# Performance work log

Measured on AMD Instinct MI355X. Metric: run time of the kernel, lower is better.

## Reference

```python
import jax, jax.numpy as jnp
import numpy as np
import math

N_EMBD = 1024
N_HEAD = 16
B, T = 2, 2048


def new_gelu(x):
    # GPT-2 tanh-approx GELU (matches torch module exactly)
    return 0.5 * x * (1.0 + jnp.tanh(jnp.sqrt(2.0 / jnp.pi) * (x + 0.044715 * x ** 3)))


def layer_norm(x, w, b, eps=1e-5):
    mu = jnp.mean(x, axis=-1, keepdims=True)
    var = jnp.var(x, axis=-1, keepdims=True)
    return (x - mu) * jax.lax.rsqrt(var + eps) * w + b


def setup_inputs() -> dict:
    key = jax.random.key(0)
    ks = jax.random.split(key, 8)
    C = N_EMBD
    s = 0.02
    return {
        "x": jax.random.normal(ks[0], (B, T, C), dtype=jnp.float32),
        "ln1_w": jnp.ones((C,), jnp.float32),
        "ln1_b": jnp.zeros((C,), jnp.float32),
        "attn_w": s * jax.random.normal(ks[1], (C, 3 * C), jnp.float32),
        "attn_b": jnp.zeros((3 * C,), jnp.float32),
        "attn_proj_w": s * jax.random.normal(ks[2], (C, C), jnp.float32),
        "attn_proj_b": jnp.zeros((C,), jnp.float32),
        "ln2_w": jnp.ones((C,), jnp.float32),
        "ln2_b": jnp.zeros((C,), jnp.float32),
        "fc_w": s * jax.random.normal(ks[3], (C, 4 * C), jnp.float32),
        "fc_b": jnp.zeros((4 * C,), jnp.float32),
        "mlp_proj_w": s * jax.random.normal(ks[4], (4 * C, C), jnp.float32),
        "mlp_proj_b": jnp.zeros((C,), jnp.float32),
    }


def block_forward(x, ln1_w, ln1_b, attn_w, attn_b, attn_proj_w, attn_proj_b,
                  ln2_w, ln2_b, fc_w, fc_b, mlp_proj_w, mlp_proj_b):
    Bm, Tm, C = x.shape
    H = N_HEAD
    D = C // H
    # --- self attention (pre-LN) ---
    h = layer_norm(x, ln1_w, ln1_b)
    qkv = h @ attn_w + attn_b  # [B,T,3C]
    q, k, v = jnp.split(qkv, 3, axis=-1)
    q = q.reshape(Bm, Tm, H, D).transpose(0, 2, 1, 3)  # [B,H,T,D]
    k = k.reshape(Bm, Tm, H, D).transpose(0, 2, 1, 3)
    v = v.reshape(Bm, Tm, H, D).transpose(0, 2, 1, 3)
    att = jnp.einsum('bhqd,bhkd->bhqk', q, k) * (1.0 / math.sqrt(D))
    att = jax.nn.softmax(att, axis=-1)  # NOTE: no causal mask in source
    y = jnp.einsum('bhqk,bhkd->bhqd', att, v)
    y = y.transpose(0, 2, 1, 3).reshape(Bm, Tm, C)
    x = x + (y @ attn_proj_w + attn_proj_b)
    # --- MLP ---
    h = layer_norm(x, ln2_w, ln2_b)
    h = new_gelu(h @ fc_w + fc_b)
    x = x + (h @ mlp_proj_w + mlp_proj_b)
    return x


def reference(x, ln1_w, ln1_b, attn_w, attn_b, attn_proj_w, attn_proj_b,
              ln2_w, ln2_b, fc_w, fc_b, mlp_proj_w, mlp_proj_b):
    return block_forward(x, ln1_w, ln1_b, attn_w, attn_b, attn_proj_w, attn_proj_b,
                         ln2_w, ln2_b, fc_w, fc_b, mlp_proj_w, mlp_proj_b)
```

## Files before the change

### kernel.cpp

```cpp
#include <hip/hip_runtime.h>

typedef __attribute__((ext_vector_type(4))) float  f32x4;
typedef __attribute__((ext_vector_type(8))) short  s16x8;
typedef __attribute__((ext_vector_type(4))) short  s16x4;

__device__ __forceinline__ short f2bf(float f) {
    unsigned u = __builtin_bit_cast(unsigned, f);
    u += 0x7fff + ((u >> 16) & 1);
    return (short)(u >> 16);
}

__device__ __forceinline__ void load_lds16(const void* g, void* l) {
    __builtin_amdgcn_global_load_lds(
        (const __attribute__((address_space(1))) unsigned int*)g,
        (__attribute__((address_space(3))) unsigned int*)l, 16, 0, 0);
}

__global__ __launch_bounds__(256) void transpose_cast(const float* __restrict__ W,
                                                      short* __restrict__ Wt,
                                                      int K, int N) {
    __shared__ float t[32][33];
    int n0 = blockIdx.x * 32, k0 = blockIdx.y * 32;
    int tx = threadIdx.x & 31, ty = threadIdx.x >> 5;
#pragma unroll
    for (int i = 0; i < 4; i++)
        t[ty + 8 * i][tx] = W[(size_t)(k0 + ty + 8 * i) * N + n0 + tx];
    __syncthreads();
#pragma unroll
    for (int i = 0; i < 4; i++)
        Wt[(size_t)(n0 + ty + 8 * i) * K + k0 + tx] = f2bf(t[tx][ty + 8 * i]);
}

__global__ __launch_bounds__(256) void vtrans_kernel(const short* __restrict__ qkv,
                                                     short* __restrict__ Vtg) {
    const int T = 2048, C3 = 3072;
    __shared__ short tl[32][33];
    int bh = blockIdx.y >> 1;
    int b = bh >> 4, h = bh & 15;
    int dh = (blockIdx.y & 1) * 32;
    int t0 = blockIdx.x * 32;
    int tx = threadIdx.x & 31, ty = threadIdx.x >> 5;
    const short* src = qkv + (size_t)b * T * C3 + 2048 + h * 64 + dh;
#pragma unroll
    for (int i = 0; i < 4; i++)
        tl[ty + 8 * i][tx] = src[(size_t)(t0 + ty + 8 * i) * C3 + tx];
    __syncthreads();
#pragma unroll
    for (int i = 0; i < 4; i++)
        Vtg[((size_t)bh * 64 + dh + ty + 8 * i) * T + t0 + tx] = tl[tx][ty + 8 * i];
}

__global__ __launch_bounds__(256) void ln_kernel(const float* __restrict__ x,
                                                 const float* __restrict__ w,
                                                 const float* __restrict__ b,
                                                 short* __restrict__ out) {
    int row = blockIdx.x;
    int tid = threadIdx.x;
    const float4 v = ((const float4*)(x + (size_t)row * 1024))[tid];
    float s  = v.x + v.y + v.z + v.w;
    float ss = v.x * v.x + v.y * v.y + v.z * v.z + v.w * v.w;
#pragma unroll
    for (int o = 32; o > 0; o >>= 1) {
        s  += __shfl_down(s, o);
        ss += __shfl_down(ss, o);
    }
    __shared__ float rs[4], rq[4];
    int wave = tid >> 6, lane = tid & 63;
    if (lane == 0) { rs[wave] = s; rq[wave] = ss; }
    __syncthreads();
    float tot = rs[0] + rs[1] + rs[2] + rs[3];
    float tq  = rq[0] + rq[1] + rq[2] + rq[3];
    float mu   = tot * (1.f / 1024.f);
    float var  = tq * (1.f / 1024.f) - mu * mu;
    float rstd = rsqrtf(var + 1e-5f);
    const float4 wv = ((const float4*)w)[tid];
    const float4 bv = ((const float4*)b)[tid];
    s16x4 o;
    o[0] = f2bf((v.x - mu) * rstd * wv.x + bv.x);
    o[1] = f2bf((v.y - mu) * rstd * wv.y + bv.y);
    o[2] = f2bf((v.z - mu) * rstd * wv.z + bv.z);
    o[3] = f2bf((v.w - mu) * rstd * wv.w + bv.w);
    ((s16x4*)(out + (size_t)row * 1024))[tid] = o;
}

template <typename OUT_T, bool GELU, bool RES, bool SCALE_Q>
__global__ __launch_bounds__(256) void gemm_bt(const short* __restrict__ A,
                                               const short* __restrict__ Bt,
                                               const float* __restrict__ bias,
                                               const float* __restrict__ res,
                                               OUT_T* __restrict__ C,
                                               int M, int N, int K) {
    __shared__ __align__(16) short As[128 * 32];
    __shared__ __align__(16) short Bs[128 * 32];
    int tid = threadIdx.x;
    int m0 = blockIdx.y * 128, n0 = blockIdx.x * 128;
    int wave = tid >> 6, lane = tid & 63;
    int wr = wave >> 1, wc = wave & 1;
    int g = lane >> 4, q = lane & 15;
    f32x4 acc[4][4] = {};
    const short* Ab = A + (size_t)m0 * K;
    const short* Bb = Bt + (size_t)n0 * K;
    int srow = tid >> 2;
    int scol = (tid & 3) * 8;
    for (int k0 = 0; k0 < K; k0 += 32) {
        __syncthreads();
        load_lds16(Ab + (size_t)srow * K + k0 + scol, As + tid * 8);
        load_lds16(Ab + (size_t)(srow + 64) * K + k0 + scol, As + 2048 + tid * 8);
        load_lds16(Bb + (size_t)srow * K + k0 + scol, Bs + tid * 8);
        load_lds16(Bb + (size_t)(srow + 64) * K + k0 + scol, Bs + 2048 + tid * 8);
        __syncthreads();
        s16x8 a[4], bf[4];
#pragma unroll
        for (int mi = 0; mi < 4; mi++)
            a[mi] = *(const s16x8*)(As + (wr * 64 + mi * 16 + q) * 32 + g * 8);
#pragma unroll
        for (int ni = 0; ni < 4; ni++)
            bf[ni] = *(const s16x8*)(Bs + (wc * 64 + ni * 16 + q) * 32 + g * 8);
#pragma unroll
        for (int mi = 0; mi < 4; mi++)
#pragma unroll
            for (int ni = 0; ni < 4; ni++)
                acc[mi][ni] = __builtin_amdgcn_mfma_f32_16x16x32_bf16(a[mi], bf[ni], acc[mi][ni], 0, 0, 0);
    }
#pragma unroll
    for (int mi = 0; mi < 4; mi++) {
#pragma unroll
        for (int ni = 0; ni < 4; ni++) {
            int row = m0 + wr * 64 + mi * 16 + g * 4;
            int col = n0 + wc * 64 + ni * 16 + q;
            float bb = bias[col];
#pragma unroll
            for (int r = 0; r < 4; r++) {
                float v = acc[mi][ni][r] + bb;
                if (RES) v += res[(size_t)(row + r) * N + col];
                if (GELU) {
                    float aa = 0.7978845608028654f * (v + 0.044715f * v * v * v);
                    float th = 1.f - 2.f / (__expf(2.f * aa) + 1.f);
                    v = 0.5f * v * (1.f + th);
                }
                if (SCALE_Q && col < 1024) v *= 0.18033688011112042f;
                if constexpr (sizeof(OUT_T) == 2)
                    C[(size_t)(row + r) * N + col] = f2bf(v);
                else
                    C[(size_t)(row + r) * N + col] = v;
            }
        }
    }
}

__global__ __launch_bounds__(256) void gemm_bt_sk(const short* __restrict__ A,
                                                  const short* __restrict__ Bt,
                                                  float* __restrict__ part,
                                                  int M, int N, int K, int Klen) {
    __shared__ __align__(16) short As[128 * 32];
    __shared__ __align__(16) short Bs[128 * 32];
    int tid = threadIdx.x;
    int m0 = blockIdx.y * 128, n0 = blockIdx.x * 128;
    int kz = blockIdx.z;
    int wave = tid >> 6, lane = tid & 63;
    int wr = wave >> 1, wc = wave & 1;
    int g = lane >> 4, q = lane & 15;
    f32x4 acc[4][4] = {};
    const short* Ab = A + (size_t)m0 * K;
    const short* Bb = Bt + (size_t)n0 * K;
    int srow = tid >> 2;
    int scol = (tid & 3) * 8;
    int kend = kz * Klen + Klen;
    for (int k0 = kz * Klen; k0 < kend; k0 += 32) {
        __syncthreads();
        load_lds16(Ab + (size_t)srow * K + k0 + scol, As + tid * 8);
        load_lds16(Ab + (size_t)(srow + 64) * K + k0 + scol, As + 2048 + tid * 8);
        load_lds16(Bb + (size_t)srow * K + k0 + scol, Bs + tid * 8);
        load_lds16(Bb + (size_t)(srow + 64) * K + k0 + scol, Bs + 2048 + tid * 8);
        __syncthreads();
        s16x8 a[4], bf[4];
#pragma unroll
        for (int mi = 0; mi < 4; mi++)
            a[mi] = *(const s16x8*)(As + (wr * 64 + mi * 16 + q) * 32 + g * 8);
#pragma unroll
        for (int ni = 0; ni < 4; ni++)
            bf[ni] = *(const s16x8*)(Bs + (wc * 64 + ni * 16 + q) * 32 + g * 8);
#pragma unroll
        for (int mi = 0; mi < 4; mi++)
#pragma unroll
            for (int ni = 0; ni < 4; ni++)
                acc[mi][ni] = __builtin_amdgcn_mfma_f32_16x16x32_bf16(a[mi], bf[ni], acc[mi][ni], 0, 0, 0);
    }
    float* pb = part + (size_t)kz * M * N;
#pragma unroll
    for (int mi = 0; mi < 4; mi++) {
#pragma unroll
        for (int ni = 0; ni < 4; ni++) {
            int row = m0 + wr * 64 + mi * 16 + g * 4;
            int col = n0 + wc * 64 + ni * 16 + q;
#pragma unroll
            for (int r = 0; r < 4; r++)
                pb[(size_t)(row + r) * N + col] = acc[mi][ni][r];
        }
    }
}

template <int SK>
__global__ __launch_bounds__(256) void reduce_sk(const float* __restrict__ part,
                                                 const float* __restrict__ bias,
                                                 const float* __restrict__ res,
                                                 float* __restrict__ out,
                                                 int MN, int N) {
    int tot = MN >> 2;
    int nb4 = (N >> 2) - 1;
    for (int i = blockIdx.x * 256 + threadIdx.x; i < tot; i += gridDim.x * 256) {
        float4 s = ((const float4*)part)[i];
#pragma unroll
        for (int k = 1; k < SK; k++) {
            float4 p = ((const float4*)(part + (size_t)k * MN))[i];
            s.x += p.x; s.y += p.y; s.z += p.z; s.w += p.w;
        }
        float4 bv = ((const float4*)bias)[i & nb4];
        float4 rv = ((const float4*)res)[i];
        float4 o;
        o.x = s.x + bv.x + rv.x;
        o.y = s.y + bv.y + rv.y;
        o.z = s.z + bv.z + rv.z;
        o.w = s.w + bv.w + rv.w;
        ((float4*)out)[i] = o;
    }
}

__global__ __launch_bounds__(256) void attn_kernel(const short* __restrict__ qkv,
                                                   const short* __restrict__ Vtg,
                                                   short* __restrict__ y) {
    const int T = 2048, C3 = 3072;
    int wg = blockIdx.x;
    int mapped = (wg & 7) * 128 + (wg >> 3);
    int bh = mapped >> 5, qt = mapped & 31;
    int b = bh >> 4, h = bh & 15;
    int tid = threadIdx.x, lane = tid & 63, wave = tid >> 6;
    int g = lane >> 4, q = lane & 15;
    const short* base = qkv + (size_t)b * T * C3;

    int qrow = qt * 64 + wave * 16 + q;
    const short* qp = base + (size_t)qrow * C3 + h * 64 + g * 8;
    s16x8 qf0 = *(const s16x8*)qp;
    s16x8 qf1 = *(const s16x8*)(qp + 32);

    __shared__ __align__(16) short Ks[2][64 * 64];
    __shared__ __align__(16) short Vs[2][64 * 64];
    __shared__ __align__(16) short Pl[4][16 * 64];

    int srow = tid >> 3, sc8 = tid & 7;
    const short* ksrc = base + 1024 + h * 64 + (size_t)srow * C3 + ((sc8 ^ (srow & 7)) << 3);
    const short* vsrc = Vtg + ((size_t)bh * 64 + srow) * T + ((sc8 ^ (srow & 7)) << 3);

    auto stage = [&](int bi, int t) {
        const short* kp = ksrc + (size_t)(t * 64) * C3;
        load_lds16(kp, &Ks[bi][tid * 8]);
        load_lds16(kp + (size_t)32 * C3, &Ks[bi][tid * 8 + 2048]);
        const short* vp = vsrc + t * 64;
        load_lds16(vp, &Vs[bi][tid * 8]);
        load_lds16(vp + (size_t)32 * T, &Vs[bi][tid * 8 + 2048]);
    };

    float mst = -INFINITY, lst = 0.f;
    f32x4 accy[4] = {};
    int sw = q & 7;
    int s2 = sw << 1;

    stage(0, 0);
    for (int t = 0; t < 32; ++t) {
        int cur = t & 1;
        __syncthreads();
        if (t < 31) stage(cur ^ 1, t + 1);
        f32x4 sc[4];
#pragma unroll
        for (int n = 0; n < 4; n++) {
            const short* kb = &Ks[cur][(16 * n + q) * 64];
            s16x8 kf0 = *(const s16x8*)(kb + ((g ^ sw) << 3));
            s16x8 kf1 = *(const s16x8*)(kb + (((g + 4) ^ sw) << 3));
            f32x4 z = {};
            z = __builtin_amdgcn_mfma_f32_16x16x32_bf16(kf0, qf0, z, 0, 0, 0);
            sc[n] = __builtin_amdgcn_mfma_f32_16x16x32_bf16(kf1, qf1, z, 0, 0, 0);
        }
        float tm = -INFINITY;
#pragma unroll
        for (int n = 0; n < 4; n++)
#pragma unroll
            for (int r = 0; r < 4; r++) tm = fmaxf(tm, sc[n][r]);
        tm = fmaxf(tm, __shfl_xor(tm, 16));
        tm = fmaxf(tm, __shfl_xor(tm, 32));
        if (!__all(tm <= mst + 8.f)) {
            float mnew = fmaxf(mst, tm);
            float alpha = exp2f(mst - mnew);
            lst *= alpha;
#pragma unroll
            for (int r = 0; r < 4; r++) {
                float ar = __shfl(alpha, 4 * g + r);
#pragma unroll
                for (int n = 0; n < 4; n++) accy[n][r] *= ar;
            }
            mst = mnew;
        }
        float p[4][4];
        float ps = 0.f;
#pragma unroll
        for (int n = 0; n < 4; n++)
#pragma unroll
            for (int r = 0; r < 4; r++) {
                p[n][r] = exp2f(sc[n][r] - mst);
                ps += p[n][r];
            }
        ps += __shfl_xor(ps, 16);
        ps += __shfl_xor(ps, 32);
        lst += ps;
#pragma unroll
        for (int n = 0; n < 4; n++) {
            unsigned w0, w1;
            asm("v_cvt_pk_bf16_f32 %0, %1, %2" : "=v"(w0) : "v"(p[n][0]), "v"(p[n][1]));
            asm("v_cvt_pk_bf16_f32 %0, %1, %2" : "=v"(w1) : "v"(p[n][2]), "v"(p[n][3]));
            unsigned long long pw = (unsigned long long)w0 | ((unsigned long long)w1 << 32);
            *(unsigned long long*)&Pl[wave][q * 64 + (((4 * n + g) ^ s2) << 2)] = pw;
        }
        s16x8 pa0 = *(const s16x8*)&Pl[wave][q * 64 + (((2 * g) ^ s2) << 2)];
        s16x8 pa1 = *(const s16x8*)&Pl[wave][q * 64 + (((8 + 2 * g) ^ s2) << 2)];
#pragma unroll
        for (int n = 0; n < 4; n++) {
            int d = 16 * n + q, vw = d & 7;
            const short* vb = &Vs[cur][d * 64];
            s16x8 v0 = *(const s16x8*)(vb + ((g ^ vw) << 3));
            s16x8 v1 = *(const s16x8*)(vb + (((g + 4) ^ vw) << 3));
            accy[n] = __builtin_amdgcn_mfma_f32_16x16x32_bf16(pa0, v0, accy[n], 0, 0, 0);
            accy[n] = __builtin_amdgcn_mfma_f32_16x16x32_bf16(pa1, v1, accy[n], 0, 0, 0);
        }
    }
    short* yb = y + ((size_t)b * T + qt * 64 + wave * 16) * 1024 + h * 64;
#pragma unroll
    for (int r = 0; r < 4; r++) {
        float linv = 1.f / __shfl(lst, 4 * g + r);
#pragma unroll
        for (int n = 0; n < 4; n++)
            yb[(size_t)(4 * g + r) * 1024 + 16 * n + q] = f2bf(accy[n][r] * linv);
    }
}

extern "C" void kernel_launch(void* const* d_in, const int* in_sizes, int n_in,
                              void* d_out, int out_size, void* d_ws, size_t ws_size,
                              hipStream_t stream) {
    const float* x           = (const float*)d_in[0];
    const float* ln1_w       = (const float*)d_in[1];
    const float* ln1_b       = (const float*)d_in[2];
    const float* attn_w      = (const float*)d_in[3];
    const float* attn_b      = (const float*)d_in[4];
    const float* attn_proj_w = (const float*)d_in[5];
    const float* attn_proj_b = (const float*)d_in[6];
    const float* ln2_w       = (const float*)d_in[7];
    const float* ln2_b       = (const float*)d_in[8];
    const float* fc_w        = (const float*)d_in[9];
    const float* fc_b        = (const float*)d_in[10];
    const float* mlp_proj_w  = (const float*)d_in[11];
    const float* mlp_proj_b  = (const float*)d_in[12];

    const int M = 4096;

    size_t off = 0;
    char* wsb = (char*)d_ws;
    auto alloc = [&](size_t bytes) {
        void* p = wsb + off;
        off += (bytes + 255) & ~(size_t)255;
        return p;
    };
    short* wt_attn  = (short*)alloc(3072ull * 1024 * 2);
    short* wt_proj  = (short*)alloc(1024ull * 1024 * 2);
    short* wt_fc    = (short*)alloc(4096ull * 1024 * 2);
    short* wt_mproj = (short*)alloc(1024ull * 4096 * 2);
    short* h1       = (short*)alloc((size_t)M * 1024 * 2);
    short* qkvb     = (short*)alloc((size_t)M * 3072 * 2);
    short* yb       = (short*)alloc((size_t)M * 1024 * 2);
    float* x1       = (float*)alloc((size_t)M * 1024 * 4);
    short* vtg      = (short*)alloc((size_t)M * 1024 * 2);
    short* h2       = qkvb;

    size_t base_off = off;
    int SK = 0;
    if (ws_size >= base_off + 4ull * M * 1024 * 4) SK = 4;
    else if (ws_size >= base_off + 2ull * M * 1024 * 4) SK = 2;
    float* part = (float*)(wsb + base_off);

    transpose_cast<<<dim3(3072 / 32, 1024 / 32), 256, 0, stream>>>(attn_w, wt_attn, 1024, 3072);
    transpose_cast<<<dim3(1024 / 32, 1024 / 32), 256, 0, stream>>>(attn_proj_w, wt_proj, 1024, 1024);
    transpose_cast<<<dim3(4096 / 32, 1024 / 32), 256, 0, stream>>>(fc_w, wt_fc, 1024, 4096);
    transpose_cast<<<dim3(1024 / 32, 4096 / 32), 256, 0, stream>>>(mlp_proj_w, wt_mproj, 4096, 1024);

    ln_kernel<<<M, 256, 0, stream>>>(x, ln1_w, ln1_b, h1);
    gemm_bt<short, false, false, true><<<dim3(3072 / 128, M / 128), 256, 0, stream>>>(
        h1, wt_attn, attn_b, nullptr, qkvb, M, 3072, 1024);
    vtrans_kernel<<<dim3(2048 / 32, 64), 256, 0, stream>>>(qkvb, vtg);
    attn_kernel<<<1024, 256, 0, stream>>>(qkvb, vtg, yb);
    gemm_bt<float, false, true, false><<<dim3(1024 / 128, M / 128), 256, 0, stream>>>(
        yb, wt_proj, attn_proj_b, x, x1, M, 1024, 1024);
    ln_kernel<<<M, 256, 0, stream>>>(x1, ln2_w, ln2_b, h1);
    gemm_bt<short, true, false, false><<<dim3(4096 / 128, M / 128), 256, 0, stream>>>(
        h1, wt_fc, fc_b, nullptr, h2, M, 4096, 1024);

    if (SK == 4) {
        gemm_bt_sk<<<dim3(1024 / 128, M / 128, 4), 256, 0, stream>>>(
            h2, wt_mproj, part, M, 1024, 4096, 1024);
        reduce_sk<4><<<2048, 256, 0, stream>>>(part, mlp_proj_b, x1, (float*)d_out, M * 1024, 1024);
    } else if (SK == 2) {
        gemm_bt_sk<<<dim3(1024 / 128, M / 128, 2), 256, 0, stream>>>(
            h2, wt_mproj, part, M, 1024, 4096, 2048);
        reduce_sk<2><<<2048, 256, 0, stream>>>(part, mlp_proj_b, x1, (float*)d_out, M * 1024, 1024);
    } else {
        gemm_bt<float, false, true, false><<<dim3(1024 / 128, M / 128), 256, 0, stream>>>(
            h2, wt_mproj, mlp_proj_b, x1, (float*)d_out, M, 1024, 4096);
    }
}
```

Measured before the change: 315.5 us.

## Rewrite attention with 32x32 MFMA tiles and register-only P transfer

Each wave now handles 32 query rows, not 16, and uses 32x32x16 bf16 MFMAs, so a block covers 128 queries and the grid halves. The scores are laid out so each lane owns one query column. That removes the cross-lane shuffles for the row max, the row sum and the rescale, and the P matrix reaches the PV MFMA through permlane32_swap instead of an LDS round-trip. K/V tiles loaded into LDS are now reused across twice as many queries, and s_setprio is raised around the MFMA bursts. The cost is higher register pressure from 16-wide accumulators and fewer workgroups, which may lower occupancy.

Measured after the change: 308.4 us. 2.3% less time.

```diff
diff --git a/kernel.cpp b/kernel.cpp
--- a/kernel.cpp
+++ b/kernel.cpp
@@ -1,8 +1,12 @@
 #include <hip/hip_runtime.h>
 
-typedef __attribute__((ext_vector_type(4))) float  f32x4;
-typedef __attribute__((ext_vector_type(8))) short  s16x8;
-typedef __attribute__((ext_vector_type(4))) short  s16x4;
+typedef __attribute__((ext_vector_type(4)))  float  f32x4;
+typedef __attribute__((ext_vector_type(16))) float  f32x16;
+typedef __attribute__((ext_vector_type(8)))  short  s16x8;
+typedef __attribute__((ext_vector_type(4)))  short  s16x4;
+typedef __attribute__((ext_vector_type(4)))  unsigned u32x4;
+typedef __attribute__((ext_vector_type(2)))  unsigned u32x2;
+typedef __attribute__((ext_vector_type(2)))  int    i32x2;
 
 __device__ __forceinline__ short f2bf(float f) {
     unsigned u = __builtin_bit_cast(unsigned, f);
@@ -231,21 +235,22 @@
                                                    short* __restrict__ y) {
     const int T = 2048, C3 = 3072;
     int wg = blockIdx.x;
-    int mapped = (wg & 7) * 128 + (wg >> 3);
-    int bh = mapped >> 5, qt = mapped & 31;
+    int mapped = (wg & 7) * 64 + (wg >> 3);
+    int bh = mapped >> 4, qt = mapped & 15;
     int b = bh >> 4, h = bh & 15;
     int tid = threadIdx.x, lane = tid & 63, wave = tid >> 6;
-    int g = lane >> 4, q = lane & 15;
+    int ql = lane & 31, hi = lane >> 5;
     const short* base = qkv + (size_t)b * T * C3;
 
-    int qrow = qt * 64 + wave * 16 + q;
-    const short* qp = base + (size_t)qrow * C3 + h * 64 + g * 8;
-    s16x8 qf0 = *(const s16x8*)qp;
-    s16x8 qf1 = *(const s16x8*)(qp + 32);
+    int qrow = qt * 128 + wave * 32 + ql;
+    const short* qp = base + (size_t)qrow * C3 + h * 64;
+    s16x8 qf[4];
+#pragma unroll
+    for (int s = 0; s < 4; s++)
+        qf[s] = *(const s16x8*)(qp + ((2 * s + hi) << 3));
 
     __shared__ __align__(16) short Ks[2][64 * 64];
     __shared__ __align__(16) short Vs[2][64 * 64];
-    __shared__ __align__(16) short Pl[4][16 * 64];
 
     int srow = tid >> 3, sc8 = tid & 7;
     const short* ksrc = base + 1024 + h * 64 + (size_t)srow * C3 + ((sc8 ^ (srow & 7)) << 3);
@@ -261,83 +266,101 @@
     };
 
     float mst = -INFINITY, lst = 0.f;
-    f32x4 accy[4] = {};
-    int sw = q & 7;
-    int s2 = sw << 1;
+    f32x16 accY0 = {}, accY1 = {};
+    int swz = ql & 7;
 
     stage(0, 0);
     for (int t = 0; t < 32; ++t) {
         int cur = t & 1;
         __syncthreads();
         if (t < 31) stage(cur ^ 1, t + 1);
-        f32x4 sc[4];
-#pragma unroll
-        for (int n = 0; n < 4; n++) {
-            const short* kb = &Ks[cur][(16 * n + q) * 64];
-            s16x8 kf0 = *(const s16x8*)(kb + ((g ^ sw) << 3));
-            s16x8 kf1 = *(const s16x8*)(kb + (((g + 4) ^ sw) << 3));
-            f32x4 z = {};
-            z = __builtin_amdgcn_mfma_f32_16x16x32_bf16(kf0, qf0, z, 0, 0, 0);
-            sc[n] = __builtin_amdgcn_mfma_f32_16x16x32_bf16(kf1, qf1, z, 0, 0, 0);
-        }
-        float tm = -INFINITY;
-#pragma unroll
-        for (int n = 0; n < 4; n++)
-#pragma unroll
-            for (int r = 0; r < 4; r++) tm = fmaxf(tm, sc[n][r]);
-        tm = fmaxf(tm, __shfl_xor(tm, 16));
+        f32x16 s0 = {}, s1 = {};
+        const short* kb0 = &Ks[cur][ql * 64];
+        const short* kb1 = &Ks[cur][(32 + ql) * 64];
+        __builtin_amdgcn_s_setprio(1);
+#pragma unroll
+        for (int s = 0; s < 4; s++) {
+            int c = ((2 * s + hi) ^ swz) << 3;
+            s16x8 k0 = *(const s16x8*)(kb0 + c);
+            s16x8 k1 = *(const s16x8*)(kb1 + c);
+            s0 = __builtin_amdgcn_mfma_f32_32x32x16_bf16(k0, qf[s], s0, 0, 0, 0);
+            s1 = __builtin_amdgcn_mfma_f32_32x32x16_bf16(k1, qf[s], s1, 0, 0, 0);
+        }
+        __builtin_amdgcn_s_setprio(0);
+        float tm = fmaxf(s0[0], s0[1]);
+#pragma unroll
+        for (int r = 2; r < 16; r++) tm = fmaxf(tm, s0[r]);
+#pragma unroll
+        for (int r = 0; r < 16; r++) tm = fmaxf(tm, s1[r]);
         tm = fmaxf(tm, __shfl_xor(tm, 32));
         if (!__all(tm <= mst + 8.f)) {
             float mnew = fmaxf(mst, tm);
             float alpha = exp2f(mst - mnew);
             lst *= alpha;
 #pragma unroll
-            for (int r = 0; r < 4; r++) {
-                float ar = __shfl(alpha, 4 * g + r);
-#pragma unroll
-                for (int n = 0; n < 4; n++) accy[n][r] *= ar;
-            }
+            for (int r = 0; r < 16; r++) { accY0[r] *= alpha; accY1[r] *= alpha; }
             mst = mnew;
         }
-        float p[4][4];
         float ps = 0.f;
 #pragma unroll
-        for (int n = 0; n < 4; n++)
-#pragma unroll
-            for (int r = 0; r < 4; r++) {
-                p[n][r] = exp2f(sc[n][r] - mst);
-                ps += p[n][r];
-            }
-        ps += __shfl_xor(ps, 16);
+        for (int r = 0; r < 16; r++) { s0[r] = exp2f(s0[r] - mst); ps += s0[r]; }
+#pragma unroll
+        for (int r = 0; r < 16; r++) { s1[r] = exp2f(s1[r] - mst); ps += s1[r]; }
         ps += __shfl_xor(ps, 32);
         lst += ps;
-#pragma unroll
-        for (int n = 0; n < 4; n++) {
-            unsigned w0, w1;
-            asm("v_cvt_pk_bf16_f32 %0, %1, %2" : "=v"(w0) : "v"(p[n][0]), "v"(p[n][1]));
-            asm("v_cvt_pk_bf16_f32 %0, %1, %2" : "=v"(w1) : "v"(p[n][2]), "v"(p[n][3]));
-            unsigned long long pw = (unsigned long long)w0 | ((unsigned long long)w1 << 32);
-            *(unsigned long long*)&Pl[wave][q * 64 + (((4 * n + g) ^ s2) << 2)] = pw;
-        }
-        s16x8 pa0 = *(const s16x8*)&Pl[wave][q * 64 + (((2 * g) ^ s2) << 2)];
-        s16x8 pa1 = *(const s16x8*)&Pl[wave][q * 64 + (((8 + 2 * g) ^ s2) << 2)];
-#pragma unroll
-        for (int n = 0; n < 4; n++) {
-            int d = 16 * n + q, vw = d & 7;
-            const short* vb = &Vs[cur][d * 64];
-            s16x8 v0 = *(const s16x8*)(vb + ((g ^ vw) << 3));
-            s16x8 v1 = *(const s16x8*)(vb + (((g + 4) ^ vw) << 3));
-            accy[n] = __builtin_amdgcn_mfma_f32_16x16x32_bf16(pa0, v0, accy[n], 0, 0, 0);
-            accy[n] = __builtin_amdgcn_mfma_f32_16x16x32_bf16(pa1, v1, accy[n], 0, 0, 0);
-        }
-    }
-    short* yb = y + ((size_t)b * T + qt * 64 + wave * 16) * 1024 + h * 64;
+        s16x8 pb[4];
+#pragma unroll
+        for (int s = 0; s < 4; s++) {
+            int tt = (s & 1) * 8;
+            unsigned lo0, lo1, hi0, hi1;
+            if (s < 2) {
+                asm("v_cvt_pk_bf16_f32 %0, %1, %2" : "=v"(lo0) : "v"(s0[tt + 0]), "v"(s0[tt + 1]));
+                asm("v_cvt_pk_bf16_f32 %0, %1, %2" : "=v"(lo1) : "v"(s0[tt + 2]), "v"(s0[tt + 3]));
+                asm("v_cvt_pk_bf16_f32 %0, %1, %2" : "=v"(hi0) : "v"(s0[tt + 4]), "v"(s0[tt + 5]));
+                asm("v_cvt_pk_bf16_f32 %0, %1, %2" : "=v"(hi1) : "v"(s0[tt + 6]), "v"(s0[tt + 7]));
+            } else {
+                asm("v_cvt_pk_bf16_f32 %0, %1, %2" : "=v"(lo0) : "v"(s1[tt + 0]), "v"(s1[tt + 1]));
+                asm("v_cvt_pk_bf16_f32 %0, %1, %2" : "=v"(lo1) : "v"(s1[tt + 2]), "v"(s1[tt + 3]));
+                asm("v_cvt_pk_bf16_f32 %0, %1, %2" : "=v"(hi0) : "v"(s1[tt + 4]), "v"(s1[tt + 5]));
+                asm("v_cvt_pk_bf16_f32 %0, %1, %2" : "=v"(hi1) : "v"(s1[tt + 6]), "v"(s1[tt + 7]));
+            }
+            i32x2 r0 = __builtin_amdgcn_permlane32_swap((int)hi0, (int)lo0, false, false);
+            i32x2 r1 = __builtin_amdgcn_permlane32_swap((int)hi1, (int)lo1, false, false);
+            u32x4 w;
+            w[0] = (unsigned)r0[1]; w[1] = (unsigned)r1[1];
+            w[2] = (unsigned)r0[0]; w[3] = (unsigned)r1[0];
+            pb[s] = __builtin_bit_cast(s16x8, w);
+        }
+        const short* vb0 = &Vs[cur][ql * 64];
+        const short* vb1 = &Vs[cur][(32 + ql) * 64];
+        __builtin_amdgcn_s_setprio(1);
+#pragma unroll
+        for (int s = 0; s < 4; s++) {
+            int c = ((2 * s + hi) ^ swz) << 3;
+            s16x8 v0 = *(const s16x8*)(vb0 + c);
+            s16x8 v1 = *(const s16x8*)(vb1 + c);
+            accY0 = __builtin_amdgcn_mfma_f32_32x32x16_bf16(v0, pb[s], accY0, 0, 0, 0);
+            accY1 = __builtin_amdgcn_mfma_f32_32x32x16_bf16(v1, pb[s], accY1, 0, 0, 0);
+        }
+        __builtin_amdgcn_s_setprio(0);
+    }
+    float linv = 1.f / lst;
+    short* yrow = y + ((size_t)b * T + qrow) * 1024 + h * 64;
 #pragma unroll
     for (int r = 0; r < 4; r++) {
-        float linv = 1.f / __shfl(lst, 4 * g + r);
-#pragma unroll
-        for (int n = 0; n < 4; n++)
-            yb[(size_t)(4 * g + r) * 1024 + 16 * n + q] = f2bf(accy[n][r] * linv);
+        unsigned w0, w1, w2, w3;
+        float a0 = accY0[4 * r] * linv, a1 = accY0[4 * r + 1] * linv;
+        float a2 = accY0[4 * r + 2] * linv, a3 = accY0[4 * r + 3] * linv;
+        float b0 = accY1[4 * r] * linv, b1 = accY1[4 * r + 1] * linv;
+        float b2 = accY1[4 * r + 2] * linv, b3 = accY1[4 * r + 3] * linv;
+        asm("v_cvt_pk_bf16_f32 %0, %1, %2" : "=v"(w0) : "v"(a0), "v"(a1));
+        asm("v_cvt_pk_bf16_f32 %0, %1, %2" : "=v"(w1) : "v"(a2), "v"(a3));
+        asm("v_cvt_pk_bf16_f32 %0, %1, %2" : "=v"(w2) : "v"(b0), "v"(b1));
+        asm("v_cvt_pk_bf16_f32 %0, %1, %2" : "=v"(w3) : "v"(b2), "v"(b3));
+        u32x2 p0; p0[0] = w0; p0[1] = w1;
+        u32x2 p1; p1[0] = w2; p1[1] = w3;
+        *(u32x2*)(yrow + 8 * r + 4 * hi)      = p0;
+        *(u32x2*)(yrow + 32 + 8 * r + 4 * hi) = p1;
     }
 }
 
@@ -393,7 +416,7 @@
     gemm_bt<short, false, false, true><<<dim3(3072 / 128, M / 128), 256, 0, stream>>>(
         h1, wt_attn, attn_b, nullptr, qkvb, M, 3072, 1024);
     vtrans_kernel<<<dim3(2048 / 32, 64), 256, 0, stream>>>(qkvb, vtg);
-    attn_kernel<<<1024, 256, 0, stream>>>(qkvb, vtg, yb);
+    attn_kernel<<<512, 256, 0, stream>>>(qkvb, vtg, yb);
     gemm_bt<float, false, true, false><<<dim3(1024 / 128, M / 128), 256, 0, stream>>>(
         yb, wt_proj, attn_proj_b, x, x1, M, 1024, 1024);
     ln_kernel<<<M, 256, 0, stream>>>(x1, ln2_w, ln2_b, h1);
```
